# Kernel tuning notes

Measured on AMD Instinct MI355X. Metric: run time of the kernel, lower is better.

Reference implementation:

```python
import jax, jax.numpy as jnp
import numpy as np
from jax import lax

B, N, F_IN, T = 1024, 22, 32, 32
K = 3
CHEV = 64     # nb_chev_filter
TIMEF = 64    # nb_time_filter
LN_EPS = 1e-5


def setup_inputs() -> dict:
    key = jax.random.key(0)
    ks = jax.random.split(key, 19)
    rn = lambda k, shape, s=0.1: (jax.random.normal(k, shape, jnp.float32) * s)
    return {
        "x": rn(ks[0], (B, N, F_IN, T), 1.0),
        # Temporal_Attention_layer params
        "U1": rn(ks[1], (N,)),
        "U2": rn(ks[2], (F_IN, N)),
        "U3": rn(ks[3], (F_IN,)),
        "be": rn(ks[4], (1, T, T)),
        "Ve": rn(ks[5], (T, T)),
        # Spatial_Attention_layer params
        "W1": rn(ks[6], (T,)),
        "W2": rn(ks[7], (F_IN, T)),
        "W3": rn(ks[8], (F_IN,)),
        "bs": rn(ks[9], (1, N, N)),
        "Vs": rn(ks[10], (N, N)),
        # cheb_conv_withSAt params
        "Theta": rn(ks[11], (K, F_IN, CHEV)),
        "node_emb": rn(ks[12], (N, N), 1.0),
        # time conv (1x3, pad (0,1)) and residual conv (1x1)
        "tconv_w": rn(ks[13], (TIMEF, CHEV, 1, 3)),
        "tconv_b": rn(ks[14], (TIMEF,)),
        "rconv_w": rn(ks[15], (TIMEF, F_IN, 1, 1)),
        "rconv_b": rn(ks[16], (TIMEF,)),
        # LayerNorm over nb_time_filter
        "ln_g": jnp.ones((TIMEF,), jnp.float32),
        "ln_b": jnp.zeros((TIMEF,), jnp.float32),
    }


def reference(x, U1, U2, U3, be, Ve, W1, W2, W3, bs, Vs, Theta, node_emb,
              tconv_w, tconv_b, rconv_w, rconv_b, ln_g, ln_b):
    Bx, Nx, Fx, Tx = x.shape

    # ---- Temporal attention: E_normalized [B, T, T] ----
    # lhs = ((x.permute(0,3,2,1) @ U1) @ U2)  -> [B, T, N]
    lhs_t = jnp.einsum('bnft,n->btf', x, U1) @ U2          # [B,T,N]
    rhs_t = jnp.einsum('f,bnft->bnt', U3, x)               # [B,N,T]
    prod_t = jnp.einsum('btn,bns->bts', lhs_t, rhs_t)      # [B,T,T]
    E = jnp.einsum('ts,bsu->btu', Ve, jax.nn.sigmoid(prod_t + be))
    E_norm = jax.nn.softmax(E, axis=1)                     # softmax over dim=1

    # x_TAt = reshape(x, [B, N*F, T]) @ E_norm  -> [B, N, F, T]
    x_TAt = (x.reshape(Bx, Nx * Fx, Tx) @ E_norm).reshape(Bx, Nx, Fx, Tx)

    # ---- Spatial attention on x_TAt: S_normalized [B, N, N] ----
    lhs_s = jnp.einsum('bnft,t->bnf', x_TAt, W1) @ W2      # [B,N,T]
    rhs_s = jnp.einsum('f,bnft->bnt', W3, x_TAt)           # [B,N,T]
    prod_s = jnp.einsum('bnt,bmt->bnm', lhs_s, rhs_s)      # [B,N,N]
    S = jnp.einsum('nm,bml->bnl', Vs, jax.nn.sigmoid(prod_s + bs))
    S_norm = jax.nn.softmax(S, axis=1)                     # softmax over dim=1

    # ---- Chebyshev graph conv with adaptive supports (vectorized over T) ----
    supports = jax.nn.softmax(jax.nn.relu(node_emb @ node_emb.T), axis=1)
    support_set = [jnp.eye(Nx, dtype=x.dtype), supports]
    for _ in range(2, K):
        support_set.append(2.0 * supports @ support_set[-1] - support_set[-2])

    out = jnp.zeros((Bx, Nx, CHEV, Tx), x.dtype)
    for k in range(K):
        A_k = support_set[k][None, :, :] * S_norm          # [B,N,N]
        # rhs[b,m,f,t] = sum_n A_k[b,n,m] * x[b,n,f,t]  (A_k^T @ graph_signal)
        rhs = jnp.einsum('bnm,bnft->bmft', A_k, x)
        out = out + jnp.einsum('bmft,fo->bmot', rhs, Theta[k])
    spatial_gcn = jax.nn.relu(out)                         # [B,N,CHEV,T]

    # ---- Temporal conv (1x3, pad (0,1)) on [B, CHEV, N, T] ----
    dn = ('NCHW', 'OIHW', 'NCHW')
    t_in = spatial_gcn.transpose(0, 2, 1, 3)               # [B,CHEV,N,T]
    t_out = lax.conv_general_dilated(t_in, tconv_w, (1, 1), ((0, 0), (1, 1)),
                                     dimension_numbers=dn)
    t_out = t_out + tconv_b[None, :, None, None]           # [B,TIMEF,N,T]

    # ---- Residual conv (1x1) on [B, F_in, N, T] ----
    r_in = x.transpose(0, 2, 1, 3)
    r_out = lax.conv_general_dilated(r_in, rconv_w, (1, 1), ((0, 0), (0, 0)),
                                     dimension_numbers=dn)
    r_out = r_out + rconv_b[None, :, None, None]           # [B,TIMEF,N,T]

    # ---- Residual add, ReLU, LayerNorm over channel dim ----
    y = jax.nn.relu(r_out + t_out).transpose(0, 3, 2, 1)   # [B,T,N,TIMEF]
    mu = jnp.mean(y, axis=-1, keepdims=True)
    var = jnp.var(y, axis=-1, keepdims=True)
    y = (y - mu) * lax.rsqrt(var + LN_EPS) * ln_g + ln_b
    return y.transpose(0, 2, 3, 1)                         # [B,N,TIMEF,T]
```

## Files before the change

### kernel.cpp

```cpp
#include <hip/hip_runtime.h>
#include <hip/hip_bf16.h>
#include <math.h>


typedef unsigned short u16;
typedef __attribute__((ext_vector_type(8))) short short8;
typedef __attribute__((ext_vector_type(4))) float f32x4;
typedef __attribute__((ext_vector_type(2))) float f32x2;

__device__ __forceinline__ float sigm(float v){ return 1.f/(1.f+expf(-v)); }

__device__ __forceinline__ u16 f2bf(float x){
  __hip_bfloat16 h = __float2bfloat16(x);
  return *reinterpret_cast<u16*>(&h);
}
__device__ __forceinline__ unsigned f2bf2(float lo, float hi){
  return (unsigned)f2bf(lo) | ((unsigned)f2bf(hi) << 16);
}

__global__ void k_sup_prep(const float* __restrict__ emb, float* __restrict__ wsT,
                           const float* __restrict__ Theta,
                           const float* __restrict__ tw, const float* __restrict__ tb,
                           const float* __restrict__ rw, const float* __restrict__ rb,
                           u16* __restrict__ thA, u16* __restrict__ wA, float* __restrict__ wsB){
  if (blockIdx.x < 81){
    int tid = blockIdx.x*256 + threadIdx.x;
    if (tid < 6144){
      int j = tid&7, l = (tid>>3)&63, blk = tid>>9;
      int ks = blk>>2, ci = blk&3, r = l&15, g = l>>4;
      int kf = 32*ks + 8*g + j, c = 16*ci + r;
      thA[tid] = f2bf(Theta[kf*64 + c]);
    } else if (tid < 20480){
      int e = tid - 6144;
      int j = e&7, l = (e>>3)&63, blk = e>>9;
      int ks = blk>>2, oi = blk&3, r = l&15, g = l>>4;
      int k = 32*ks + 8*g + j, o = 16*oi + r;
      float v = (k < 192) ? tw[o*192 + (k&63)*3 + (k>>6)] : rw[o*32 + (k-192)];
      wA[e] = f2bf(v);
    } else if (tid < 20544){
      int o = tid - 20480; wsB[o] = tb[o] + rb[o];
    }
    return;
  }
  __shared__ float M[484];
  __shared__ float T1s[484];
  int tid = threadIdx.x;
  for (int idx=tid; idx<484; idx+=256){
    int n = idx/22, m = idx - (idx/22)*22;
    float s = 0.f;
    for (int j=0;j<22;j++) s += emb[n*22+j]*emb[m*22+j];
    M[idx] = fmaxf(s, 0.f);
  }
  __syncthreads();
  if (tid < 22){
    float mx = -1e30f;
    for (int m=0;m<22;m++) mx = fmaxf(mx, M[tid*22+m]);
    float s = 0.f;
    for (int m=0;m<22;m++) s += expf(M[tid*22+m]-mx);
    float inv = 1.f/s;
    for (int m=0;m<22;m++) T1s[tid*22+m] = expf(M[tid*22+m]-mx)*inv;
  }
  __syncthreads();
  for (int idx=tid; idx<484; idx+=256){
    int n = idx/22, m = idx - (idx/22)*22;
    float s = 0.f;
    for (int p=0;p<22;p++) s += T1s[n*22+p]*T1s[p*22+m];
    wsT[idx]      = T1s[idx];
    wsT[484+idx]  = 2.f*s - ((n==m)?1.f:0.f);
  }
}

__global__ __launch_bounds__(512) void k_attn(
    const float* __restrict__ x,
    const float* __restrict__ U1, const float* __restrict__ U2, const float* __restrict__ U3,
    const float* __restrict__ be, const float* __restrict__ Ve,
    const float* __restrict__ W1, const float* __restrict__ W2, const float* __restrict__ W3,
    const float* __restrict__ bs, const float* __restrict__ Vs,
    float* __restrict__ snorm){
  int b = blockIdx.x, tid = threadIdx.x;
  const float* xb = x + (size_t)b*22528;
  __shared__ float xu1[1024];
  __shared__ float rhs_t[704];
  __shared__ float lhs_t[704];
  __shared__ float sigp[1024];
  __shared__ float Em[1024];
  __shared__ float sm[1024];
  __shared__ float w1e[32];
  __shared__ float xw3[704];
  __shared__ float lhsS[704];
  __shared__ float lhs2[704];
  __shared__ float rhsS[704];
  __shared__ float sig2[484];
  __shared__ float Sl[484];

  {
    int idx = tid*2;
    f32x2 a = {0.f, 0.f};
    #pragma unroll 2
    for (int n=0;n<22;n++){
      f32x2 xv = *(const f32x2*)&xb[n*1024 + idx];
      float u = U1[n];
      a[0] = fmaf(xv[0], u, a[0]);
      a[1] = fmaf(xv[1], u, a[1]);
    }
    *(f32x2*)&xu1[idx] = a;
  }
  if (tid < 352){
    int n = tid>>4, t = (tid&15)*2;
    f32x2 a = {0.f,0.f}, c = {0.f,0.f};
    #pragma unroll 4
    for (int f=0;f<32;f++){
      f32x2 xv = *(const f32x2*)&xb[n*1024 + f*32 + t];
      float u3 = U3[f], w3 = W3[f];
      a[0] = fmaf(u3, xv[0], a[0]); a[1] = fmaf(u3, xv[1], a[1]);
      c[0] = fmaf(w3, xv[0], c[0]); c[1] = fmaf(w3, xv[1], c[1]);
    }
    *(f32x2*)&rhs_t[n*32+t] = a;
    *(f32x2*)&xw3[n*32+t]   = c;
  }
  __syncthreads();
  if (tid < 352){
    int t = tid&31, np = tid>>5;
    int n2 = np*2;
    f32x2 a = {0.f,0.f};
    #pragma unroll 4
    for (int f=0;f<32;f++){
      float bc = xu1[f*32+t];
      f32x2 u2 = *(const f32x2*)&U2[f*22+n2];
      a[0] = fmaf(bc, u2[0], a[0]); a[1] = fmaf(bc, u2[1], a[1]);
    }
    *(f32x2*)&lhs_t[t*22+n2] = a;
  }
  __syncthreads();
  {
    int s = tid>>4, u = (tid&15)*2;
    f32x2 p = {0.f,0.f};
    #pragma unroll 2
    for (int n=0;n<22;n++){
      float lv = lhs_t[s*22+n];
      f32x2 rv = *(const f32x2*)&rhs_t[n*32+u];
      p[0] = fmaf(lv, rv[0], p[0]); p[1] = fmaf(lv, rv[1], p[1]);
    }
    f32x2 be2 = *(const f32x2*)&be[s*32+u];
    sigp[s*32+u]   = sigm(p[0] + be2[0]);
    sigp[s*32+u+1] = sigm(p[1] + be2[1]);
  }
  __syncthreads();
  {
    int t = tid>>4, u = (tid&15)*2;
    f32x2 a = {0.f,0.f};
    #pragma unroll 4
    for (int s2=0;s2<32;s2++){
      float vv = Ve[t*32+s2];
      f32x2 sp = *(const f32x2*)&sigp[s2*32+u];
      a[0] = fmaf(vv, sp[0], a[0]); a[1] = fmaf(vv, sp[1], a[1]);
    }
    *(f32x2*)&Em[t*32+u] = a;
  }
  __syncthreads();
  {
    int u = tid>>4, th = tid&15;
    float e0 = Em[(2*th)*32 + u], e1 = Em[(2*th+1)*32 + u];
    float mx = fmaxf(e0, e1);
    #pragma unroll
    for (int mask=1; mask<16; mask<<=1) mx = fmaxf(mx, __shfl_xor(mx, mask));
    float x0 = expf(e0-mx), x1 = expf(e1-mx);
    float s = x0 + x1;
    #pragma unroll
    for (int mask=1; mask<16; mask<<=1) s += __shfl_xor(s, mask);
    float inv = 1.f/s;
    sm[(2*th)*32 + u]   = x0*inv;
    sm[(2*th+1)*32 + u] = x1*inv;
  }
  __syncthreads();
  {
    int u = tid>>4, th = tid&15;
    float pw = fmaf(sm[u*32 + 2*th], W1[2*th], sm[u*32 + 2*th+1]*W1[2*th+1]);
    #pragma unroll
    for (int mask=1; mask<16; mask<<=1) pw += __shfl_xor(pw, mask);
    if (th==0) w1e[u] = pw;
  }
  __syncthreads();
  for (int idx=tid; idx<704; idx+=512){
    int n = idx>>5, f = idx&31;
    const float4* xp = (const float4*)(xb + n*1024 + f*32);
    const float4* wv = (const float4*)w1e;
    float a = 0.f;
    #pragma unroll
    for (int q=0;q<8;q++){
      float4 xv = xp[q], w4 = wv[q];
      a = fmaf(xv.x, w4.x, a); a = fmaf(xv.y, w4.y, a);
      a = fmaf(xv.z, w4.z, a); a = fmaf(xv.w, w4.w, a);
    }
    lhsS[idx]=a;
  }
  __syncthreads();
  if (tid < 352){
    int n = tid>>4, t = (tid&15)*2;
    f32x2 a = {0.f,0.f};
    #pragma unroll 4
    for (int f=0;f<32;f++){
      float lv = lhsS[n*32+f];
      f32x2 w2 = *(const f32x2*)&W2[f*32+t];
      a[0] = fmaf(lv, w2[0], a[0]); a[1] = fmaf(lv, w2[1], a[1]);
    }
    *(f32x2*)&lhs2[n*32+t] = a;
  }
  if (tid < 352){
    int mm = tid>>4, t = (tid&15)*2;
    f32x2 a = {0.f,0.f};
    #pragma unroll 4
    for (int u=0;u<32;u++){
      float xv = xw3[mm*32+u];
      f32x2 smv = *(const f32x2*)&sm[u*32+t];
      a[0] = fmaf(xv, smv[0], a[0]); a[1] = fmaf(xv, smv[1], a[1]);
    }
    *(f32x2*)&rhsS[mm*32+t] = a;
  }
  __syncthreads();
  if (tid < 484){
    int a_ = tid/22, l = tid - (tid/22)*22;
    const float4* lp = (const float4*)&lhs2[a_*32];
    const float4* rp = (const float4*)&rhsS[l*32];
    float p = 0.f;
    #pragma unroll
    for (int q=0;q<8;q++){
      float4 lv = lp[q], rv = rp[q];
      p = fmaf(lv.x, rv.x, p); p = fmaf(lv.y, rv.y, p);
      p = fmaf(lv.z, rv.z, p); p = fmaf(lv.w, rv.w, p);
    }
    sig2[tid] = sigm(p + bs[tid]);
  }
  __syncthreads();
  {
    int n = tid>>4, lp_ = tid&15;
    if (n < 22 && lp_ < 11){
      int l = lp_*2;
      f32x2 s = {0.f,0.f};
      #pragma unroll 2
      for (int mm=0;mm<22;mm++){
        float vv = Vs[n*22+mm];
        f32x2 sg = *(const f32x2*)&sig2[mm*22+l];
        s[0] = fmaf(vv, sg[0], s[0]); s[1] = fmaf(vv, sg[1], s[1]);
      }
      *(f32x2*)&Sl[n*22+l] = s;
    }
  }
  __syncthreads();
  {
    int grp = tid>>5, nn = tid&31;
    for (int l = grp; l < 22; l += 16){
      float v = (nn<22) ? Sl[nn*22 + l] : -1e30f;
      float mx = v;
      #pragma unroll
      for (int mask=1; mask<32; mask<<=1) mx = fmaxf(mx, __shfl_xor(mx, mask));
      float e = (nn<22) ? expf(v-mx) : 0.f;
      float s = e;
      #pragma unroll
      for (int mask=1; mask<32; mask<<=1) s += __shfl_xor(s, mask);
      if (nn<22) snorm[(size_t)b*484 + nn*22 + l] = e*(1.f/s);
    }
  }
}

__global__ __launch_bounds__(256, 6) void k_fused(
    const float* __restrict__ x,
    const float* __restrict__ wsT, const float* __restrict__ snorm,
    const u16* __restrict__ thA, const u16* __restrict__ wA, const float* __restrict__ wsB,
    const float* __restrict__ lng, const float* __restrict__ lnb,
    float* __restrict__ out){
  __shared__ __align__(16) u16 GtU[2][32*72];
  __shared__ __align__(16) u16 sgTU[2][34*72];
  __shared__ __align__(16) u16 xTU[2][32*40];
  __shared__ __align__(16) float ak4[22*4];
  __shared__ float smm[2];

  int wg = blockIdx.x;
  int logical = (wg & 7)*1408 + (wg >> 3);
  int b = logical/11, mp = logical - b*11;
  int m0 = mp*2;
  int tid = threadIdx.x;
  const float* xb = x + (size_t)b*22528;

  if (tid < 128){
    int mi = tid>>6, r6 = tid&63;
    int row = (r6>>5) ? 33 : 0, c2 = r6&31;
    *(unsigned*)&sgTU[mi][row*72 + c2*2] = 0u;
  }
  if (tid < 88){
    int n = tid>>2, j = tid&3;
    int mi = j>>1, k1 = j&1;
    int m = m0 + mi;
    ak4[tid] = wsT[k1*484 + n*22 + m] * snorm[(size_t)b*484 + n*22 + m];
  }
  if (tid < 2) smm[tid] = snorm[(size_t)b*484 + (m0+tid)*23];
  __syncthreads();

  {
    f32x2 acc[4][2];
    #pragma unroll
    for (int j=0;j<4;j++){ acc[j][0]=f32x2{0,0}; acc[j][1]=f32x2{0,0}; }
    const float4* x4 = (const float4*)xb;
    #pragma unroll 2
    for (int n=0;n<22;n++){
      float4 av = *(const float4*)&ak4[n*4];
      float4 xv = x4[n*256 + tid];
      f32x2 xlo = {xv.x, xv.y}, xhi2 = {xv.z, xv.w};
      f32x2 c0 = {av.x,av.x}, c1 = {av.y,av.y}, c2 = {av.z,av.z}, c3 = {av.w,av.w};
      acc[0][0] = __builtin_elementwise_fma(c0, xlo,  acc[0][0]);
      acc[0][1] = __builtin_elementwise_fma(c0, xhi2, acc[0][1]);
      acc[1][0] = __builtin_elementwise_fma(c1, xlo,  acc[1][0]);
      acc[1][1] = __builtin_elementwise_fma(c1, xhi2, acc[1][1]);
      acc[2][0] = __builtin_elementwise_fma(c2, xlo,  acc[2][0]);
      acc[2][1] = __builtin_elementwise_fma(c2, xhi2, acc[2][1]);
      acc[3][0] = __builtin_elementwise_fma(c3, xlo,  acc[3][0]);
      acc[3][1] = __builtin_elementwise_fma(c3, xhi2, acc[3][1]);
    }
    int f = tid>>3, t7 = tid&7, t0 = t7*4;
    int w4 = f>>3, f_low = f&7;
    int gcol0 = 8*((0*4 + w4) ^ t7) + f_low;
    int gcol1 = 8*((1*4 + w4) ^ t7) + f_low;
    int xcol  = 8*(w4 ^ (t7&3)) + f_low;
    #pragma unroll
    for (int mi=0;mi<2;mi++){
      float4 xm = ((const float4*)xb)[(m0+mi)*256 + tid];
      u16* xd = &xTU[mi][0];
      xd[(t0+0)*40 + xcol] = f2bf(xm.x);
      xd[(t0+1)*40 + xcol] = f2bf(xm.y);
      xd[(t0+2)*40 + xcol] = f2bf(xm.z);
      xd[(t0+3)*40 + xcol] = f2bf(xm.w);
      #pragma unroll
      for (int k1=0;k1<2;k1++){
        int j = mi*2 + k1;
        int gc = k1 ? gcol1 : gcol0;
        u16* gd = &GtU[mi][gc];
        gd[(t0+0)*72] = f2bf(acc[j][0][0]);
        gd[(t0+1)*72] = f2bf(acc[j][0][1]);
        gd[(t0+2)*72] = f2bf(acc[j][1][0]);
        gd[(t0+3)*72] = f2bf(acc[j][1][1]);
      }
    }
  }
  __syncthreads();

  int w = tid>>6, l = tid&63, r = l&15, g = l>>4;

  {
    const u16* tA = thA + (size_t)(w*64 + l)*8;
    short8 a0 = *(const short8*)(tA);
    short8 a1 = *(const short8*)(tA + 2048);
    short8 a2 = *(const short8*)(tA + 4096);
    #pragma unroll
    for (int mi=0;mi<2;mi++){
      float sm_ = smm[mi];
      #pragma unroll
      for (int ti=0; ti<2; ++ti){
        int row = ti*16 + r;
        int h  = (row>>2)&7;
        int h2 = (row>>2)&3;
        f32x4 a12 = {0.f,0.f,0.f,0.f}, ax = {0.f,0.f,0.f,0.f};
        const u16* gp0 = &GtU[mi][row*72 + 8*((0*4+g)^h)];
        const u16* gp1 = &GtU[mi][row*72 + 8*((1*4+g)^h)];
        a12 = __builtin_amdgcn_mfma_f32_16x16x32_bf16(a1, *(const short8*)(gp0), a12, 0,0,0);
        a12 = __builtin_amdgcn_mfma_f32_16x16x32_bf16(a2, *(const short8*)(gp1), a12, 0,0,0);
        const u16* xp = &xTU[mi][row*40 + 8*(g^h2)];
        ax  = __builtin_amdgcn_mfma_f32_16x16x32_bf16(a0, *(const short8*)(xp),  ax,  0,0,0);
        int orow = 1 + row, c0 = w*16 + g*4;
        float v0 = fmaxf(fmaf(sm_, ax[0], a12[0]), 0.f);
        float v1 = fmaxf(fmaf(sm_, ax[1], a12[1]), 0.f);
        float v2 = fmaxf(fmaf(sm_, ax[2], a12[2]), 0.f);
        float v3 = fmaxf(fmaf(sm_, ax[3], a12[3]), 0.f);
        *(unsigned*)&sgTU[mi][orow*72 + c0]     = f2bf2(v0, v1);
        *(unsigned*)&sgTU[mi][orow*72 + c0 + 2] = f2bf2(v2, v3);
      }
    }
  }
  __syncthreads();

  f32x4 acc[2][2];
  acc[0][0]=f32x4{0,0,0,0}; acc[0][1]=f32x4{0,0,0,0};
  acc[1][0]=f32x4{0,0,0,0}; acc[1][1]=f32x4{0,0,0,0};
  {
    const u16* pA = wA + (size_t)(w*64 + l)*8;
    #pragma unroll
    for (int ks=0; ks<6; ++ks){
      short8 wk = *(const short8*)(pA + ks*2048);
      int seg = ks>>1, colb = (ks&1)*32 + 8*g;
      #pragma unroll
      for (int mi=0;mi<2;mi++){
        const u16* q0 = &sgTU[mi][(r + seg)*72 + colb];
        acc[mi][0] = __builtin_amdgcn_mfma_f32_16x16x32_bf16(wk, *(const short8*)(q0),         acc[mi][0], 0,0,0);
        acc[mi][1] = __builtin_amdgcn_mfma_f32_16x16x32_bf16(wk, *(const short8*)(q0 + 16*72), acc[mi][1], 0,0,0);
      }
    }
    short8 wk = *(const short8*)(pA + 6*2048);
    int h2 = (r>>2)&3;
    #pragma unroll
    for (int mi=0;mi<2;mi++){
      const u16* q = &xTU[mi][r*40 + 8*(g^h2)];
      acc[mi][0] = __builtin_amdgcn_mfma_f32_16x16x32_bf16(wk, *(const short8*)(q),         acc[mi][0], 0,0,0);
      acc[mi][1] = __builtin_amdgcn_mfma_f32_16x16x32_bf16(wk, *(const short8*)(q + 16*40), acc[mi][1], 0,0,0);
    }
  }

  float4 bias4 = ((const float4*)wsB)[w*4 + g];
  float bb[4] = {bias4.x, bias4.y, bias4.z, bias4.w};
  float y[2][2][4];
  float s1[2][2] = {{0.f,0.f},{0.f,0.f}}, s2[2][2] = {{0.f,0.f},{0.f,0.f}};
  #pragma unroll
  for (int mi=0;mi<2;mi++){
    #pragma unroll
    for (int h=0;h<2;h++){
      #pragma unroll
      for (int i=0;i<4;i++){
        float v = fmaxf(acc[mi][h][i] + bb[i], 0.f);
        y[mi][h][i] = v;
        s1[mi][h] += v;
        s2[mi][h] = fmaf(v, v, s2[mi][h]);
      }
      s1[mi][h] += __shfl_xor(s1[mi][h],16); s1[mi][h] += __shfl_xor(s1[mi][h],32);
      s2[mi][h] += __shfl_xor(s2[mi][h],16); s2[mi][h] += __shfl_xor(s2[mi][h],32);
    }
  }
  float* p1 = (float*)&GtU[0][0];
  float* p2 = p1 + 256;
  if (l < 16){
    #pragma unroll
    for (int mi=0;mi<2;mi++){
      p1[(mi*32 + l)*4 + w]      = s1[mi][0];
      p1[(mi*32 + 16 + l)*4 + w] = s1[mi][1];
      p2[(mi*32 + l)*4 + w]      = s2[mi][0];
      p2[(mi*32 + 16 + l)*4 + w] = s2[mi][1];
    }
  }
  __syncthreads();
  float4 g4 = ((const float4*)lng)[w*4 + g];
  float4 b4 = ((const float4*)lnb)[w*4 + g];
  float gg[4]={g4.x,g4.y,g4.z,g4.w}, bgg[4]={b4.x,b4.y,b4.z,b4.w};
  #pragma unroll
  for (int mi=0;mi<2;mi++){
    float4 q1a = ((const float4*)p1)[mi*32 + r],      q2a = ((const float4*)p2)[mi*32 + r];
    float4 q1b = ((const float4*)p1)[mi*32 + 16 + r], q2b = ((const float4*)p2)[mi*32 + 16 + r];
    float S1a = q1a.x+q1a.y+q1a.z+q1a.w, S2a = q2a.x+q2a.y+q2a.z+q2a.w;
    float S1b = q1b.x+q1b.y+q1b.z+q1b.w, S2b = q2b.x+q2b.y+q2b.z+q2b.w;
    float mu0 = S1a*(1.f/64.f), var0 = S2a*(1.f/64.f) - mu0*mu0, rs0 = rsqrtf(var0 + 1e-5f);
    float mu1 = S1b*(1.f/64.f), var1 = S2b*(1.f/64.f) - mu1*mu1, rs1 = rsqrtf(var1 + 1e-5f);
    float* ob = out + ((size_t)(b*22 + m0 + mi)*64 + (w*16 + g*4))*32;
    #pragma unroll
    for (int i=0;i<4;i++){
      ob[i*32 + r]      = (y[mi][0][i]-mu0)*rs0*gg[i] + bgg[i];
      ob[i*32 + 16 + r] = (y[mi][1][i]-mu1)*rs1*gg[i] + bgg[i];
    }
  }
}

extern "C" void kernel_launch(void* const* d_in, const int* in_sizes, int n_in,
                              void* d_out, int out_size, void* d_ws, size_t ws_size,
                              hipStream_t stream){
  const float* x     = (const float*)d_in[0];
  const float* U1    = (const float*)d_in[1];
  const float* U2    = (const float*)d_in[2];
  const float* U3    = (const float*)d_in[3];
  const float* be    = (const float*)d_in[4];
  const float* Ve    = (const float*)d_in[5];
  const float* W1    = (const float*)d_in[6];
  const float* W2    = (const float*)d_in[7];
  const float* W3    = (const float*)d_in[8];
  const float* bs    = (const float*)d_in[9];
  const float* Vs    = (const float*)d_in[10];
  const float* Theta = (const float*)d_in[11];
  const float* emb   = (const float*)d_in[12];
  const float* tw    = (const float*)d_in[13];
  const float* tb    = (const float*)d_in[14];
  const float* rw    = (const float*)d_in[15];
  const float* rb    = (const float*)d_in[16];
  const float* lng   = (const float*)d_in[17];
  const float* lnb   = (const float*)d_in[18];
  float* out = (float*)d_out;
  float* wsf = (float*)d_ws;
  float* wsT   = wsf;
  float* snorm = wsf + 1024;
  u16*   thA   = (u16*)(wsf + 496640);
  u16*   wA    = (u16*)(wsf + 499712);
  float* wsB   = wsf + 506880;

  k_sup_prep<<<82, 256, 0, stream>>>(emb, wsT, Theta, tw, tb, rw, rb, thA, wA, wsB);
  k_attn<<<1024, 512, 0, stream>>>(x, U1,U2,U3, be,Ve, W1,W2,W3, bs,Vs, snorm);
  k_fused<<<1024*11, 256, 0, stream>>>(x, wsT, snorm, thA, wA, wsB, lng, lnb, out);
}
```

Baseline: 157.9 us.

## Load x slice into registers once and reuse across attention reductions

k_attn now loads each thread's slice of x (22 f32x2 values) into registers once. It reuses them for the U1 reduction, the U3/W3 reductions (done with shuffles plus a shared-memory partial-sum buffer), and the W1-weighted reduction. This replaces three separate global reads of x. It also adds a launch-bounds occupancy hint of 4. The cost is higher register pressure, a new 22KB shared buffer that may reduce occupancy, and extra barriers.

```diff
diff --git a/kernel.cpp b/kernel.cpp
--- a/kernel.cpp
+++ b/kernel.cpp
@@ -70,7 +70,7 @@
   }
 }
 
-__global__ __launch_bounds__(512) void k_attn(
+__global__ __launch_bounds__(512, 4) void k_attn(
     const float* __restrict__ x,
     const float* __restrict__ U1, const float* __restrict__ U2, const float* __restrict__ U3,
     const float* __restrict__ be, const float* __restrict__ Ve,
@@ -92,41 +92,69 @@
   __shared__ float rhsS[704];
   __shared__ float sig2[484];
   __shared__ float Sl[484];
-
-  {
-    int idx = tid*2;
-    f32x2 a = {0.f, 0.f};
-    #pragma unroll 2
+  __shared__ __align__(16) float4 part[1408];
+
+  int f = tid>>4, tp = tid&15, w8 = tid>>6;
+
+  f32x2 xr[22];
+  #pragma unroll
+  for (int n=0;n<22;n++) xr[n] = *(const f32x2*)&xb[n*1024 + f*32 + 2*tp];
+
+  {
+    f32x2 a = {0.f,0.f};
+    #pragma unroll
     for (int n=0;n<22;n++){
-      f32x2 xv = *(const f32x2*)&xb[n*1024 + idx];
       float u = U1[n];
-      a[0] = fmaf(xv[0], u, a[0]);
-      a[1] = fmaf(xv[1], u, a[1]);
-    }
-    *(f32x2*)&xu1[idx] = a;
-  }
-  if (tid < 352){
-    int n = tid>>4, t = (tid&15)*2;
-    f32x2 a = {0.f,0.f}, c = {0.f,0.f};
-    #pragma unroll 4
-    for (int f=0;f<32;f++){
-      f32x2 xv = *(const f32x2*)&xb[n*1024 + f*32 + t];
-      float u3 = U3[f], w3 = W3[f];
-      a[0] = fmaf(u3, xv[0], a[0]); a[1] = fmaf(u3, xv[1], a[1]);
-      c[0] = fmaf(w3, xv[0], c[0]); c[1] = fmaf(w3, xv[1], c[1]);
-    }
-    *(f32x2*)&rhs_t[n*32+t] = a;
-    *(f32x2*)&xw3[n*32+t]   = c;
-  }
-  __syncthreads();
+      a[0] = fmaf(xr[n][0], u, a[0]);
+      a[1] = fmaf(xr[n][1], u, a[1]);
+    }
+    *(f32x2*)&xu1[f*32 + 2*tp] = a;
+  }
+
+  {
+    float u3 = U3[f], w3v = W3[f];
+    #pragma unroll
+    for (int c=0;c<2;c++){
+      #pragma unroll
+      for (int j=0;j<11;j++){
+        int n = c*11 + j;
+        float rx = xr[n][0]*u3,  ry = xr[n][1]*u3;
+        float wx = xr[n][0]*w3v, wy = xr[n][1]*w3v;
+        rx += __shfl_xor(rx,16); rx += __shfl_xor(rx,32);
+        ry += __shfl_xor(ry,16); ry += __shfl_xor(ry,32);
+        wx += __shfl_xor(wx,16); wx += __shfl_xor(wx,32);
+        wy += __shfl_xor(wy,16); wy += __shfl_xor(wy,32);
+        if ((tid&63) < 16){
+          float4 v; v.x=rx; v.y=ry; v.z=wx; v.w=wy;
+          part[(w8*11 + j)*16 + tp] = v;
+        }
+      }
+      __syncthreads();
+      if (tid < 352){
+        int nl = tid>>5, t = tid&31;
+        int tpp = t>>1, lh = t&1;
+        float sr = 0.f, sw = 0.f;
+        #pragma unroll
+        for (int w=0;w<8;w++){
+          float4 v = part[(w*11 + nl)*16 + tpp];
+          sr += lh ? v.y : v.x;
+          sw += lh ? v.w : v.z;
+        }
+        rhs_t[(c*11+nl)*32 + t] = sr;
+        xw3 [(c*11+nl)*32 + t] = sw;
+      }
+      __syncthreads();
+    }
+  }
+
   if (tid < 352){
     int t = tid&31, np = tid>>5;
     int n2 = np*2;
     f32x2 a = {0.f,0.f};
     #pragma unroll 4
-    for (int f=0;f<32;f++){
-      float bc = xu1[f*32+t];
-      f32x2 u2 = *(const f32x2*)&U2[f*22+n2];
+    for (int ff=0;ff<32;ff++){
+      float bc = xu1[ff*32+t];
+      f32x2 u2 = *(const f32x2*)&U2[ff*22+n2];
       a[0] = fmaf(bc, u2[0], a[0]); a[1] = fmaf(bc, u2[1], a[1]);
     }
     *(f32x2*)&lhs_t[t*22+n2] = a;
@@ -181,27 +209,24 @@
     if (th==0) w1e[u] = pw;
   }
   __syncthreads();
-  for (int idx=tid; idx<704; idx+=512){
-    int n = idx>>5, f = idx&31;
-    const float4* xp = (const float4*)(xb + n*1024 + f*32);
-    const float4* wv = (const float4*)w1e;
-    float a = 0.f;
-    #pragma unroll
-    for (int q=0;q<8;q++){
-      float4 xv = xp[q], w4 = wv[q];
-      a = fmaf(xv.x, w4.x, a); a = fmaf(xv.y, w4.y, a);
-      a = fmaf(xv.z, w4.z, a); a = fmaf(xv.w, w4.w, a);
-    }
-    lhsS[idx]=a;
+  {
+    f32x2 wv = *(const f32x2*)&w1e[2*tp];
+    #pragma unroll
+    for (int n=0;n<22;n++){
+      float s = fmaf(xr[n][0], wv[0], xr[n][1]*wv[1]);
+      s += __shfl_xor(s,1); s += __shfl_xor(s,2);
+      s += __shfl_xor(s,4); s += __shfl_xor(s,8);
+      if (tp == 0) lhsS[n*32 + f] = s;
+    }
   }
   __syncthreads();
   if (tid < 352){
     int n = tid>>4, t = (tid&15)*2;
     f32x2 a = {0.f,0.f};
     #pragma unroll 4
-    for (int f=0;f<32;f++){
-      float lv = lhsS[n*32+f];
-      f32x2 w2 = *(const f32x2*)&W2[f*32+t];
+    for (int ff=0;ff<32;ff++){
+      float lv = lhsS[n*32+ff];
+      f32x2 w2 = *(const f32x2*)&W2[ff*32+t];
       a[0] = fmaf(lv, w2[0], a[0]); a[1] = fmaf(lv, w2[1], a[1]);
     }
     *(f32x2*)&lhs2[n*32+t] = a;
@@ -316,8 +341,8 @@
       acc[3][0] = __builtin_elementwise_fma(c3, xlo,  acc[3][0]);
       acc[3][1] = __builtin_elementwise_fma(c3, xhi2, acc[3][1]);
     }
-    int f = tid>>3, t7 = tid&7, t0 = t7*4;
-    int w4 = f>>3, f_low = f&7;
+    int ff = tid>>3, t7 = tid&7, t0 = t7*4;
+    int w4 = ff>>3, f_low = ff&7;
     int gcol0 = 8*((0*4 + w4) ^ t7) + f_low;
     int gcol1 = 8*((1*4 + w4) ^ t7) + f_low;
     int xcol  = 8*(w4 ^ (t7&3)) + f_low;
```

Measured after the change: 158.7 us. About the same (+0.5%).
